# Optimization experiments

Measured on AMD Instinct MI355X. Metric: run time of the kernel, lower is better.

Reference implementation:

```python
import jax, jax.numpy as jnp
import numpy as np

D_MODEL = 1024
NUM_HEADS = 16
MAX_LEN = 500
D_K = D_MODEL // NUM_HEADS


def setup_inputs() -> dict:
    key = jax.random.key(0)
    ks = jax.random.split(key, 10)
    B, L = 8, 500
    s = 1.0 / np.sqrt(D_MODEL)
    return {
        "query": jax.random.normal(ks[0], (B, L, D_MODEL), dtype=jnp.float32),
        "key": jax.random.normal(ks[1], (B, L, D_MODEL), dtype=jnp.float32),
        "value": jax.random.normal(ks[2], (B, L, D_MODEL), dtype=jnp.float32),
        "Wq": jax.random.normal(ks[3], (D_MODEL, D_MODEL), dtype=jnp.float32) * s,
        "bq": jnp.zeros((D_MODEL,), dtype=jnp.float32),
        "Wk": jax.random.normal(ks[4], (D_MODEL, D_MODEL), dtype=jnp.float32) * s,
        "bk": jnp.zeros((D_MODEL,), dtype=jnp.float32),
        "Wv": jax.random.normal(ks[5], (D_MODEL, D_MODEL), dtype=jnp.float32) * s,
        "bv": jnp.zeros((D_MODEL,), dtype=jnp.float32),
        "rel_emb": jax.random.normal(ks[6], (NUM_HEADS, 2 * MAX_LEN - 1), dtype=jnp.float32),
    }


def reference(query, key, value, Wq, bq, Wk, bk, Wv, bv, rel_emb):
    B, Lq, _ = query.shape
    Lk = key.shape[1]
    H, dk = NUM_HEADS, D_K
    # QKV projections -> [B, H, L, d]
    q = (query @ Wq + bq).reshape(B, Lq, H, dk).transpose(0, 2, 1, 3)
    k = (key @ Wk + bk).reshape(B, Lk, H, dk).transpose(0, 2, 1, 3)
    v = (value @ Wv + bv).reshape(B, Lk, H, dk).transpose(0, 2, 1, 3)
    scores = jnp.einsum('bhqd,bhkd->bhqk', q, k) / jnp.sqrt(jnp.float32(dk))
    # gathered relative-position bias: [H, Lq, Lk]
    rel_idx = jnp.arange(Lq)[:, None] - jnp.arange(Lk)[None, :] + MAX_LEN - 1
    bias = rel_emb[:, rel_idx]  # [H, Lq, Lk]
    scores = scores + bias[None]
    attn = jax.nn.softmax(scores, axis=-1)
    out = jnp.einsum('bhqk,bhkd->bhqd', attn, v)
    return out.transpose(0, 2, 1, 3).reshape(B, Lq, H * dk)
```

## Files before the change

### kernel.cpp

```cpp
#include <hip/hip_runtime.h>

typedef short bf16x8 __attribute__((ext_vector_type(8)));
typedef float f32x4 __attribute__((ext_vector_type(4)));
typedef unsigned uint4v __attribute__((ext_vector_type(4)));

#define B_    8
#define L_    500
#define LP    512
#define H_    16
#define DK    64
#define DM    1024
#define MP    4096
#define NT    8

static __device__ __forceinline__ unsigned short f2bf(float x) {
  unsigned u = __float_as_uint(x);
  u += 0x7fffu + ((u >> 16) & 1u);
  return (unsigned short)(u >> 16);
}

static __device__ __forceinline__ unsigned cvtpk(float lo, float hi) {
  unsigned r;
  asm("v_cvt_pk_bf16_f32 %0, %1, %2" : "=v"(r) : "v"(lo), "v"(hi));
  return r;
}

static __device__ __forceinline__ void gload16(const void* g, void* l) {
  __builtin_amdgcn_global_load_lds(
      (const __attribute__((address_space(1))) void*)g,
      (__attribute__((address_space(3))) void*)l, 16, 0, 0);
}

static __device__ __forceinline__ f32x4 MF(bf16x8 a, bf16x8 b, f32x4 c) {
  return __builtin_amdgcn_mfma_f32_16x16x32_bf16(a, b, c, 0, 0, 0);
}

__global__ __launch_bounds__(256) void conv_kernel(
    const float* __restrict__ iq, const float* __restrict__ ik,
    const float* __restrict__ iv,
    const float* __restrict__ wq, const float* __restrict__ wk,
    const float* __restrict__ wv,
    unsigned short* __restrict__ X, unsigned short* __restrict__ Wt) {
  const int z = blockIdx.y;
  const int bx = blockIdx.x;
  const int tid = threadIdx.x;
  if (bx < 2048) {
    const float* src = (z == 0) ? iq : (z == 1) ? ik : iv;
    const size_t off = ((size_t)bx * 256 + tid) * 8;
    const int m = (int)(off >> 10);
    unsigned short o[8];
    if (m < 4000) {
      const float4 a = *(const float4*)(src + off);
      const float4 b = *(const float4*)(src + off + 4);
      o[0]=f2bf(a.x); o[1]=f2bf(a.y); o[2]=f2bf(a.z); o[3]=f2bf(a.w);
      o[4]=f2bf(b.x); o[5]=f2bf(b.y); o[6]=f2bf(b.z); o[7]=f2bf(b.w);
    } else {
#pragma unroll
      for (int i = 0; i < 8; ++i) o[i] = 0;
    }
    uint4 pk;
    pk.x = (unsigned)o[0] | ((unsigned)o[1] << 16);
    pk.y = (unsigned)o[2] | ((unsigned)o[3] << 16);
    pk.z = (unsigned)o[4] | ((unsigned)o[5] << 16);
    pk.w = (unsigned)o[6] | ((unsigned)o[7] << 16);
    *(uint4*)(X + (size_t)z * MP * DM + off) = pk;
    return;
  }
  const int bw = bx - 2048;
  const float* W = (z == 0) ? wq : (z == 1) ? wk : wv;
  const int k0 = (bw >> 4) * 64;
  const int n0 = (bw & 15) * 64;
  __shared__ float t[64][65];
  const int row = tid >> 2;
  const int cb  = (tid & 3) * 16;
#pragma unroll
  for (int s = 0; s < 4; ++s) {
    const float4 v = *(const float4*)(W + (size_t)(k0 + row) * DM + n0 + cb + s * 4);
    t[row][cb + s * 4 + 0] = v.x; t[row][cb + s * 4 + 1] = v.y;
    t[row][cb + s * 4 + 2] = v.z; t[row][cb + s * 4 + 3] = v.w;
  }
  __syncthreads();
  const int nr = tid >> 2;
  const int kb = (tid & 3) * 16;
#pragma unroll
  for (int s = 0; s < 2; ++s) {
    unsigned short o[8];
#pragma unroll
    for (int e = 0; e < 8; ++e) o[e] = f2bf(t[kb + s * 8 + e][nr]);
    uint4 pk;
    pk.x = (unsigned)o[0] | ((unsigned)o[1] << 16);
    pk.y = (unsigned)o[2] | ((unsigned)o[3] << 16);
    pk.z = (unsigned)o[4] | ((unsigned)o[5] << 16);
    pk.w = (unsigned)o[6] | ((unsigned)o[7] << 16);
    *(uint4*)(Wt + (size_t)z * DM * DM + (size_t)(n0 + nr) * DM + k0 + kb + s * 8) = pk;
  }
}

__global__ __launch_bounds__(256) void gemm_qkv_kernel(
    const unsigned short* __restrict__ X, const unsigned short* __restrict__ Wt,
    const float* __restrict__ bq, const float* __restrict__ bk,
    const float* __restrict__ bv,
    unsigned short* __restrict__ qo, unsigned short* __restrict__ ko,
    unsigned short* __restrict__ vo) {
  const int z = blockIdx.y;
  const unsigned short* A  = X  + (size_t)z * MP * DM;
  const unsigned short* Bw = Wt + (size_t)z * DM * DM;
  const float* bias = (z == 0) ? bq : (z == 1) ? bk : bv;
  unsigned short* out = (z == 0) ? qo : (z == 1) ? ko : vo;

  const int bid = blockIdx.x;
  const int xg = bid & 7, y = bid >> 3;
  const int tm = xg + 8 * (y >> 3);
  const int tn = y & 7;
  const int tid = threadIdx.x;
  const int lane = tid & 63, wid = tid >> 6;
  const int wr = wid >> 1, wc = wid & 1;
  const int lg = lane >> 4, lr = lane & 15;

  __shared__ __attribute__((aligned(16))) unsigned short sA[3][128 * 32];
  __shared__ __attribute__((aligned(16))) unsigned short sB[3][128 * 32];

  const int c0 = tid, c1 = tid + 256;
  const int ar0 = c0 >> 2, ak0 = (c0 & 3) * 8;
  const int ar1 = c1 >> 2, ak1 = (c1 & 3) * 8;
  const unsigned short* Ab = A  + (size_t)tm * 128 * DM;
  const unsigned short* Bb = Bw + (size_t)tn * 128 * DM;

  auto STAGE = [&](int t) {
    const int buf = t % 3;
    const int kn = t * 32;
    gload16(Ab + (size_t)ar0 * DM + kn + ak0, &sA[buf][c0 * 8]);
    gload16(Ab + (size_t)ar1 * DM + kn + ak1, &sA[buf][c1 * 8]);
    gload16(Bb + (size_t)ar0 * DM + kn + ak0, &sB[buf][c0 * 8]);
    gload16(Bb + (size_t)ar1 * DM + kn + ak1, &sB[buf][c1 * 8]);
  };

  f32x4 acc[4][4];
#pragma unroll
  for (int i = 0; i < 4; ++i)
#pragma unroll
    for (int j = 0; j < 4; ++j) acc[i][j] = (f32x4){0.f, 0.f, 0.f, 0.f};

  STAGE(0); STAGE(1);
  asm volatile("s_waitcnt vmcnt(4)" ::: "memory");
  __builtin_amdgcn_s_barrier();
  __builtin_amdgcn_sched_barrier(0);

  for (int t = 0; t < 32; ++t) {
    if (t < 30) STAGE(t + 2);
    const int cb = t % 3;
    bf16x8 af[4], bfr[4];
#pragma unroll
    for (int s = 0; s < 4; ++s) {
      af[s]  = *(const bf16x8*)&sA[cb][(wr * 64 + s * 16 + lr) * 32 + lg * 8];
      bfr[s] = *(const bf16x8*)&sB[cb][(wc * 64 + s * 16 + lr) * 32 + lg * 8];
    }
#pragma unroll
    for (int i = 0; i < 4; ++i)
#pragma unroll
      for (int j = 0; j < 4; ++j)
        acc[i][j] = MF(af[i], bfr[j], acc[i][j]);
    if (t < 31) {
      if (t < 30) asm volatile("s_waitcnt vmcnt(4)" ::: "memory");
      else        asm volatile("s_waitcnt vmcnt(0)" ::: "memory");
      __builtin_amdgcn_s_barrier();
      __builtin_amdgcn_sched_barrier(0);
    }
  }

  const int nbase = tn * 128 + wc * 64 + lr;
  float bias4[4];
#pragma unroll
  for (int ns = 0; ns < 4; ++ns) bias4[ns] = bias[nbase + ns * 16];

#pragma unroll
  for (int ms = 0; ms < 4; ++ms) {
#pragma unroll
    for (int r = 0; r < 4; ++r) {
      const int m = tm * 128 + wr * 64 + ms * 16 + lg * 4 + r;
      if (m < 4000) {
        const unsigned batch = (unsigned)m / 500u;
        const int lrow = m - (int)batch * 500;
#pragma unroll
        for (int ns = 0; ns < 4; ++ns) {
          const int n = nbase + ns * 16;
          const int hh = n >> 6, d = n & 63;
          out[(((size_t)batch * H_ + hh) * LP + lrow) * DK + d] =
              f2bf(acc[ms][ns][r] + bias4[ns]);
        }
      }
    }
  }
}

__global__ __launch_bounds__(256) void transpose_v_kernel(
    const unsigned short* __restrict__ v, unsigned short* __restrict__ vt) {
  const int bh = blockIdx.y;
  const int l0 = blockIdx.x * 64;
  __shared__ unsigned short t[64][72];
  const int tid = threadIdx.x;
  const int lrw = tid >> 2, dc = (tid & 3) * 16;
  const int gl = l0 + lrw;
  if (gl < L_) {
    *(uint4*)&t[lrw][dc]     = *(const uint4*)(v + ((size_t)bh * LP + gl) * DK + dc);
    *(uint4*)&t[lrw][dc + 8] = *(const uint4*)(v + ((size_t)bh * LP + gl) * DK + dc + 8);
  } else {
    const uint4 zz = {0u, 0u, 0u, 0u};
    *(uint4*)&t[lrw][dc]     = zz;
    *(uint4*)&t[lrw][dc + 8] = zz;
  }
  __syncthreads();
  const int dr = tid >> 2, lcb = (tid & 3) * 16;
#pragma unroll
  for (int s = 0; s < 2; ++s) {
    unsigned short e[8];
#pragma unroll
    for (int i = 0; i < 8; ++i) e[i] = t[lcb + s * 8 + i][dr];
    uint4 o;
    o.x = (unsigned)e[0] | ((unsigned)e[1] << 16);
    o.y = (unsigned)e[2] | ((unsigned)e[3] << 16);
    o.z = (unsigned)e[4] | ((unsigned)e[5] << 16);
    o.w = (unsigned)e[6] | ((unsigned)e[7] << 16);
    *(uint4*)(vt + ((size_t)bh * DK + dr) * LP + l0 + lcb + s * 8) = o;
  }
}

__global__ __launch_bounds__(256, 4) void attn_kernel(
    const unsigned short* __restrict__ q, const unsigned short* __restrict__ k,
    const unsigned short* __restrict__ vt, const float* __restrict__ rel,
    float* __restrict__ out) {
  const int id = blockIdx.x;
  const int bh = id & 127, qc = id >> 7;
  const int b = bh >> 4, h = bh & 15;
  const int tid = threadIdx.x;
  const int lane = tid & 63, wid = tid >> 6;
  const int lg = lane >> 4, lr = lane & 15;

  __shared__ unsigned short kt[2][2][64][32];
  __shared__ unsigned short vtt[2][2][64][32];
  __shared__ float relb[576];

  const float LOG2E = 1.44269504f;
  const float SC = 0.125f * LOG2E;
  const int rbase = qc * 64 - 12;
  for (int i = tid; i < 575; i += 256) {
    int idx = rbase + i;
    idx = idx < 0 ? 0 : (idx > 998 ? 998 : idx);
    relb[i] = rel[h * 999 + idx] * LOG2E;
  }

  const int qrow = qc * 64 + wid * 16 + lr;
  const unsigned short* qp = q + ((size_t)bh * LP + qrow) * DK + lg * 8;
  const bf16x8 qf0 = *(const bf16x8*)qp;
  const bf16x8 qf1 = *(const bf16x8*)(qp + 32);

  const int kj = tid >> 2, dc = (tid & 3) * 16;
  const unsigned short* kgp = k + ((size_t)bh * LP + kj) * DK + dc;
  unsigned short* kls = &kt[0][dc >> 5][kj][dc & 31];
  const int vd = tid >> 2, vkg = (tid & 3) * 16;
  const unsigned short* vgp = vt + ((size_t)bh * DK + vd) * LP + vkg;
  unsigned short* vls = &vtt[0][vkg >> 5][vd][vkg & 31];

  const int sig0 = 8 * (lr >> 2) + (lr & 3);
  const int qin = wid * 16 + lr;

  f32x4 o[4];
#pragma unroll
  for (int d = 0; d < 4; ++d) o[d] = (f32x4){0.f, 0.f, 0.f, 0.f};
  float mrun = -1e30f, lrun = 0.f;

  uint4 ka0 = *(const uint4*)(kgp);
  uint4 ka1 = *(const uint4*)(kgp + 8);
  uint4 va0 = *(const uint4*)(vgp);
  uint4 va1 = *(const uint4*)(vgp + 8);

  for (int t = 0; t < NT; ++t) {
    const int buf = t & 1;
    *(uint4*)(kls + buf * 4096)     = ka0;
    *(uint4*)(kls + buf * 4096 + 8) = ka1;
    *(uint4*)(vls + buf * 4096)     = va0;
    *(uint4*)(vls + buf * 4096 + 8) = va1;
    __syncthreads();

    if (t < NT - 1) {
      const size_t ko_ = (size_t)(t + 1) * 64 * DK;
      ka0 = *(const uint4*)(kgp + ko_);
      ka1 = *(const uint4*)(kgp + ko_ + 8);
      va0 = *(const uint4*)(vgp + (t + 1) * 64);
      va1 = *(const uint4*)(vgp + (t + 1) * 64 + 8);
    }

    f32x4 s[2][2];
#pragma unroll
    for (int kc = 0; kc < 2; ++kc)
#pragma unroll
      for (int hf = 0; hf < 2; ++hf) {
        const int sg = kc * 32 + hf * 4 + sig0;
        const bf16x8 a0 = *(const bf16x8*)&kt[buf][0][sg][lg * 8];
        const bf16x8 a1 = *(const bf16x8*)&kt[buf][1][sg][lg * 8];
        f32x4 ss = (f32x4){0.f, 0.f, 0.f, 0.f};
        ss = __builtin_amdgcn_mfma_f32_16x16x32_bf16(a0, qf0, ss, 0, 0, 0);
        ss = __builtin_amdgcn_mfma_f32_16x16x32_bf16(a1, qf1, ss, 0, 0, 0);
        s[kc][hf] = ss;
      }

    float sc[2][2][4];
#pragma unroll
    for (int kc = 0; kc < 2; ++kc)
#pragma unroll
      for (int hf = 0; hf < 2; ++hf) {
        const int bidx = qin - (t * 64 + kc * 32 + 8 * lg + 4 * hf) + 511;
#pragma unroll
        for (int r = 0; r < 4; ++r)
          sc[kc][hf][r] = s[kc][hf][r] * SC + relb[bidx - r];
      }
    if (t == NT - 1) {
#pragma unroll
      for (int hf = 0; hf < 2; ++hf)
#pragma unroll
        for (int r = 0; r < 4; ++r)
          if (8 * lg + 4 * hf + r >= 20) sc[1][hf][r] = -1e30f;
    }

    float m0 = fmaxf(fmaxf(sc[0][0][0], sc[0][0][1]), fmaxf(sc[0][0][2], sc[0][0][3]));
    float m1 = fmaxf(fmaxf(sc[0][1][0], sc[0][1][1]), fmaxf(sc[0][1][2], sc[0][1][3]));
    float m2 = fmaxf(fmaxf(sc[1][0][0], sc[1][0][1]), fmaxf(sc[1][0][2], sc[1][0][3]));
    float m3 = fmaxf(fmaxf(sc[1][1][0], sc[1][1][1]), fmaxf(sc[1][1][2], sc[1][1][3]));
    const float mloc = fmaxf(fmaxf(m0, m1), fmaxf(m2, m3));
    if (!__all(mloc - mrun <= 11.5f)) {
      float mx = fmaxf(mloc, mrun);
      mx = fmaxf(mx, __shfl_xor(mx, 16));
      mx = fmaxf(mx, __shfl_xor(mx, 32));
      const float alpha = exp2f(mrun - mx);
      mrun = mx;
      lrun *= alpha;
#pragma unroll
      for (int d = 0; d < 4; ++d) {
        o[d][0] *= alpha; o[d][1] *= alpha; o[d][2] *= alpha; o[d][3] *= alpha;
      }
    }

    float rs = 0.f;
    unsigned pw[2][4];
#pragma unroll
    for (int kc = 0; kc < 2; ++kc)
#pragma unroll
      for (int hf = 0; hf < 2; ++hf) {
        float p0 = exp2f(sc[kc][hf][0] - mrun);
        float p1 = exp2f(sc[kc][hf][1] - mrun);
        float p2 = exp2f(sc[kc][hf][2] - mrun);
        float p3 = exp2f(sc[kc][hf][3] - mrun);
        rs += (p0 + p1) + (p2 + p3);
        pw[kc][hf * 2 + 0] = cvtpk(p0, p1);
        pw[kc][hf * 2 + 1] = cvtpk(p2, p3);
      }
    rs += __shfl_xor(rs, 16);
    rs += __shfl_xor(rs, 32);
    lrun += rs;

#pragma unroll
    for (int kc = 0; kc < 2; ++kc) {
      union { uint4v u; bf16x8 v; } cv;
      cv.u = (uint4v){pw[kc][0], pw[kc][1], pw[kc][2], pw[kc][3]};
      const bf16x8 pf = cv.v;
#pragma unroll
      for (int db = 0; db < 4; ++db) {
        const bf16x8 vf = *(const bf16x8*)&vtt[buf][kc][db * 16 + lr][lg * 8];
        o[db] = __builtin_amdgcn_mfma_f32_16x16x32_bf16(vf, pf, o[db], 0, 0, 0);
      }
    }
  }

  if (qrow < L_) {
    const float inv = 1.0f / lrun;
    float* op = out + ((size_t)b * L_ + qrow) * DM + h * DK + lg * 4;
#pragma unroll
    for (int db = 0; db < 4; ++db) {
      float4 v;
      v.x = o[db][0] * inv; v.y = o[db][1] * inv;
      v.z = o[db][2] * inv; v.w = o[db][3] * inv;
      *(float4*)(op + db * 16) = v;
    }
  }
}

extern "C" void kernel_launch(void* const* d_in, const int* in_sizes, int n_in,
                              void* d_out, int out_size, void* d_ws, size_t ws_size,
                              hipStream_t stream) {
  const float* iq  = (const float*)d_in[0];
  const float* ik  = (const float*)d_in[1];
  const float* iv  = (const float*)d_in[2];
  const float* wq  = (const float*)d_in[3];
  const float* bq  = (const float*)d_in[4];
  const float* wk  = (const float*)d_in[5];
  const float* bk  = (const float*)d_in[6];
  const float* wv  = (const float*)d_in[7];
  const float* bv  = (const float*)d_in[8];
  const float* rel = (const float*)d_in[9];
  float* out = (float*)d_out;

  char* w = (char*)d_ws;
  unsigned short* X   = (unsigned short*)(w);
  unsigned short* Wt  = (unsigned short*)(w + 25165824);
  unsigned short* qb  = (unsigned short*)(w + 31457280);
  unsigned short* kb  = (unsigned short*)(w + 39845888);
  unsigned short* vb  = (unsigned short*)(w + 48234496);
  unsigned short* vtb = (unsigned short*)(w + 56623104);

  conv_kernel<<<dim3(2304, 3), 256, 0, stream>>>(iq, ik, iv, wq, wk, wv, X, Wt);
  gemm_qkv_kernel<<<dim3(256, 3), 256, 0, stream>>>(X, Wt, bq, bk, bv, qb, kb, vb);
  transpose_v_kernel<<<dim3(8, 128), 256, 0, stream>>>(vb, vtb);
  attn_kernel<<<1024, 256, 0, stream>>>(qb, kb, vtb, rel, out);
}
```

Measured before the change: 88.99 us.

## Unroll GEMM ring buffer by three and double attention query tile per block

```diff
diff --git a/kernel.cpp b/kernel.cpp
--- a/kernel.cpp
+++ b/kernel.cpp
@@ -96,6 +96,31 @@
   }
 }
 
+#define GSTEP(T_, BUF_, NBUF_)                                                    \
+  {                                                                               \
+    if ((T_) < 30) {                                                              \
+      const int kn_ = ((T_) + 2) * 32;                                            \
+      gload16(gA0 + kn_, &sA[NBUF_][c0 * 8]);                                     \
+      gload16(gA1 + kn_, &sA[NBUF_][c1 * 8]);                                     \
+      gload16(gB0 + kn_, &sB[NBUF_][c0 * 8]);                                     \
+      gload16(gB1 + kn_, &sB[NBUF_][c1 * 8]);                                     \
+    }                                                                             \
+    bf16x8 af[4], bfr[4];                                                         \
+    _Pragma("unroll") for (int s = 0; s < 4; ++s) {                               \
+      af[s]  = *(const bf16x8*)&sA[BUF_][(wr * 64 + s * 16 + lr) * 32 + lg * 8];  \
+      bfr[s] = *(const bf16x8*)&sB[BUF_][(wc * 64 + s * 16 + lr) * 32 + lg * 8];  \
+    }                                                                             \
+    _Pragma("unroll") for (int i = 0; i < 4; ++i)                                 \
+      _Pragma("unroll") for (int j = 0; j < 4; ++j)                               \
+        acc[i][j] = MF(af[i], bfr[j], acc[i][j]);                                 \
+    if ((T_) < 31) {                                                              \
+      if ((T_) < 30) asm volatile("s_waitcnt vmcnt(4)" ::: "memory");             \
+      else           asm volatile("s_waitcnt vmcnt(0)" ::: "memory");             \
+      __builtin_amdgcn_s_barrier();                                               \
+      __builtin_amdgcn_sched_barrier(0);                                          \
+    }                                                                             \
+  }
+
 __global__ __launch_bounds__(256) void gemm_qkv_kernel(
     const unsigned short* __restrict__ X, const unsigned short* __restrict__ Wt,
     const float* __restrict__ bq, const float* __restrict__ bk,
@@ -125,15 +150,10 @@
   const int ar1 = c1 >> 2, ak1 = (c1 & 3) * 8;
   const unsigned short* Ab = A  + (size_t)tm * 128 * DM;
   const unsigned short* Bb = Bw + (size_t)tn * 128 * DM;
-
-  auto STAGE = [&](int t) {
-    const int buf = t % 3;
-    const int kn = t * 32;
-    gload16(Ab + (size_t)ar0 * DM + kn + ak0, &sA[buf][c0 * 8]);
-    gload16(Ab + (size_t)ar1 * DM + kn + ak1, &sA[buf][c1 * 8]);
-    gload16(Bb + (size_t)ar0 * DM + kn + ak0, &sB[buf][c0 * 8]);
-    gload16(Bb + (size_t)ar1 * DM + kn + ak1, &sB[buf][c1 * 8]);
-  };
+  const unsigned short* gA0 = Ab + (size_t)ar0 * DM + ak0;
+  const unsigned short* gA1 = Ab + (size_t)ar1 * DM + ak1;
+  const unsigned short* gB0 = Bb + (size_t)ar0 * DM + ak0;
+  const unsigned short* gB1 = Bb + (size_t)ar1 * DM + ak1;
 
   f32x4 acc[4][4];
 #pragma unroll
@@ -141,32 +161,25 @@
 #pragma unroll
     for (int j = 0; j < 4; ++j) acc[i][j] = (f32x4){0.f, 0.f, 0.f, 0.f};
 
-  STAGE(0); STAGE(1);
+  gload16(gA0, &sA[0][c0 * 8]);
+  gload16(gA1, &sA[0][c1 * 8]);
+  gload16(gB0, &sB[0][c0 * 8]);
+  gload16(gB1, &sB[0][c1 * 8]);
+  gload16(gA0 + 32, &sA[1][c0 * 8]);
+  gload16(gA1 + 32, &sA[1][c1 * 8]);
+  gload16(gB0 + 32, &sB[1][c0 * 8]);
+  gload16(gB1 + 32, &sB[1][c1 * 8]);
   asm volatile("s_waitcnt vmcnt(4)" ::: "memory");
   __builtin_amdgcn_s_barrier();
   __builtin_amdgcn_sched_barrier(0);
 
-  for (int t = 0; t < 32; ++t) {
-    if (t < 30) STAGE(t + 2);
-    const int cb = t % 3;
-    bf16x8 af[4], bfr[4];
-#pragma unroll
-    for (int s = 0; s < 4; ++s) {
-      af[s]  = *(const bf16x8*)&sA[cb][(wr * 64 + s * 16 + lr) * 32 + lg * 8];
-      bfr[s] = *(const bf16x8*)&sB[cb][(wc * 64 + s * 16 + lr) * 32 + lg * 8];
-    }
-#pragma unroll
-    for (int i = 0; i < 4; ++i)
-#pragma unroll
-      for (int j = 0; j < 4; ++j)
-        acc[i][j] = MF(af[i], bfr[j], acc[i][j]);
-    if (t < 31) {
-      if (t < 30) asm volatile("s_waitcnt vmcnt(4)" ::: "memory");
-      else        asm volatile("s_waitcnt vmcnt(0)" ::: "memory");
-      __builtin_amdgcn_s_barrier();
-      __builtin_amdgcn_sched_barrier(0);
-    }
-  }
+  for (int t = 0; t < 30; t += 3) {
+    GSTEP(t,     0, 2);
+    GSTEP(t + 1, 1, 0);
+    GSTEP(t + 2, 2, 1);
+  }
+  GSTEP(30, 0, 2);
+  GSTEP(31, 1, 0);
 
   const int nbase = tn * 128 + wc * 64 + lr;
   float bias4[4];
@@ -225,7 +238,7 @@
   }
 }
 
-__global__ __launch_bounds__(256, 4) void attn_kernel(
+__global__ __launch_bounds__(512, 2) void attn_kernel(
     const unsigned short* __restrict__ q, const unsigned short* __restrict__ k,
     const unsigned short* __restrict__ vt, const float* __restrict__ rel,
     float* __restrict__ out) {
@@ -238,26 +251,26 @@
 
   __shared__ unsigned short kt[2][2][64][32];
   __shared__ unsigned short vtt[2][2][64][32];
-  __shared__ float relb[576];
+  __shared__ float relb[640];
 
   const float LOG2E = 1.44269504f;
   const float SC = 0.125f * LOG2E;
-  const int rbase = qc * 64 - 12;
-  for (int i = tid; i < 575; i += 256) {
+  const int rbase = qc * 128 - 12;
+  for (int i = tid; i < 639; i += 512) {
     int idx = rbase + i;
     idx = idx < 0 ? 0 : (idx > 998 ? 998 : idx);
     relb[i] = rel[h * 999 + idx] * LOG2E;
   }
 
-  const int qrow = qc * 64 + wid * 16 + lr;
+  const int qrow = qc * 128 + wid * 16 + lr;
   const unsigned short* qp = q + ((size_t)bh * LP + qrow) * DK + lg * 8;
   const bf16x8 qf0 = *(const bf16x8*)qp;
   const bf16x8 qf1 = *(const bf16x8*)(qp + 32);
 
-  const int kj = tid >> 2, dc = (tid & 3) * 16;
-  const unsigned short* kgp = k + ((size_t)bh * LP + kj) * DK + dc;
-  unsigned short* kls = &kt[0][dc >> 5][kj][dc & 31];
-  const int vd = tid >> 2, vkg = (tid & 3) * 16;
+  const int kj = tid >> 3, dcs = (tid & 7) * 8;
+  const unsigned short* kgp = k + ((size_t)bh * LP + kj) * DK + dcs;
+  unsigned short* kls = &kt[0][dcs >> 5][kj][dcs & 31];
+  const int vd = tid >> 3, vkg = (tid & 7) * 8;
   const unsigned short* vgp = vt + ((size_t)bh * DK + vd) * LP + vkg;
   unsigned short* vls = &vtt[0][vkg >> 5][vd][vkg & 31];
 
@@ -270,24 +283,17 @@
   float mrun = -1e30f, lrun = 0.f;
 
   uint4 ka0 = *(const uint4*)(kgp);
-  uint4 ka1 = *(const uint4*)(kgp + 8);
   uint4 va0 = *(const uint4*)(vgp);
-  uint4 va1 = *(const uint4*)(vgp + 8);
 
   for (int t = 0; t < NT; ++t) {
     const int buf = t & 1;
-    *(uint4*)(kls + buf * 4096)     = ka0;
-    *(uint4*)(kls + buf * 4096 + 8) = ka1;
-    *(uint4*)(vls + buf * 4096)     = va0;
-    *(uint4*)(vls + buf * 4096 + 8) = va1;
+    *(uint4*)(kls + buf * 4096) = ka0;
+    *(uint4*)(vls + buf * 4096) = va0;
     __syncthreads();
 
     if (t < NT - 1) {
-      const size_t ko_ = (size_t)(t + 1) * 64 * DK;
-      ka0 = *(const uint4*)(kgp + ko_);
-      ka1 = *(const uint4*)(kgp + ko_ + 8);
+      ka0 = *(const uint4*)(kgp + (size_t)(t + 1) * 64 * DK);
       va0 = *(const uint4*)(vgp + (t + 1) * 64);
-      va1 = *(const uint4*)(vgp + (t + 1) * 64 + 8);
     }
 
     f32x4 s[2][2];
@@ -410,5 +416,5 @@
   conv_kernel<<<dim3(2304, 3), 256, 0, stream>>>(iq, ik, iv, wq, wk, wv, X, Wt);
   gemm_qkv_kernel<<<dim3(256, 3), 256, 0, stream>>>(X, Wt, bq, bk, bv, qb, kb, vb);
   transpose_v_kernel<<<dim3(8, 128), 256, 0, stream>>>(vb, vtb);
-  attn_kernel<<<1024, 256, 0, stream>>>(qb, kb, vtb, rel, out);
-}
+  attn_kernel<<<512, 512, 0, stream>>>(qb, kb, vtb, rel, out);
+}
```

Result: slower. 95.23 us (+7.0%).

## Fuse V transpose into QKV GEMM epilogue and enlarge attention blocks

Applied to the files above, without the earlier changes.

```diff
diff --git a/kernel.cpp b/kernel.cpp
--- a/kernel.cpp
+++ b/kernel.cpp
@@ -40,7 +40,8 @@
     const float* __restrict__ iv,
     const float* __restrict__ wq, const float* __restrict__ wk,
     const float* __restrict__ wv,
-    unsigned short* __restrict__ X, unsigned short* __restrict__ Wt) {
+    unsigned short* __restrict__ X, unsigned short* __restrict__ Wt,
+    unsigned short* __restrict__ vt) {
   const int z = blockIdx.y;
   const int bx = blockIdx.x;
   const int tid = threadIdx.x;
@@ -66,6 +67,16 @@
     *(uint4*)(X + (size_t)z * MP * DM + off) = pk;
     return;
   }
+  if (bx >= 2304) {
+    if (z == 0) {
+      const int idx = (bx - 2304) * 256 + tid;
+      unsigned short* p = vt + (size_t)idx * LP + 496;
+      const uint4 zz = {0u, 0u, 0u, 0u};
+      *(uint4*)(p)     = zz;
+      *(uint4*)(p + 8) = zz;
+    }
+    return;
+  }
   const int bw = bx - 2048;
   const float* W = (z == 0) ? wq : (z == 1) ? wk : wv;
   const int k0 = (bw >> 4) * 64;
@@ -173,59 +184,49 @@
 #pragma unroll
   for (int ns = 0; ns < 4; ++ns) bias4[ns] = bias[nbase + ns * 16];
 
-#pragma unroll
-  for (int ms = 0; ms < 4; ++ms) {
-#pragma unroll
-    for (int r = 0; r < 4; ++r) {
-      const int m = tm * 128 + wr * 64 + ms * 16 + lg * 4 + r;
-      if (m < 4000) {
-        const unsigned batch = (unsigned)m / 500u;
-        const int lrow = m - (int)batch * 500;
+  if (z == 2) {
+#pragma unroll
+    for (int ms = 0; ms < 4; ++ms) {
+      const int m0 = tm * 128 + wr * 64 + ms * 16 + lg * 4;
+      if (m0 < 4000) {
+        const unsigned batch = (unsigned)m0 / 500u;
+        const int lrow0 = m0 - (int)batch * 500;
 #pragma unroll
         for (int ns = 0; ns < 4; ++ns) {
           const int n = nbase + ns * 16;
           const int hh = n >> 6, d = n & 63;
-          out[(((size_t)batch * H_ + hh) * LP + lrow) * DK + d] =
-              f2bf(acc[ms][ns][r] + bias4[ns]);
+          uint2 pk;
+          pk.x = (unsigned)f2bf(acc[ms][ns][0] + bias4[ns]) |
+                 ((unsigned)f2bf(acc[ms][ns][1] + bias4[ns]) << 16);
+          pk.y = (unsigned)f2bf(acc[ms][ns][2] + bias4[ns]) |
+                 ((unsigned)f2bf(acc[ms][ns][3] + bias4[ns]) << 16);
+          *(uint2*)(out + (((size_t)batch * H_ + hh) * DK + d) * LP + lrow0) = pk;
         }
       }
     }
-  }
-}
-
-__global__ __launch_bounds__(256) void transpose_v_kernel(
-    const unsigned short* __restrict__ v, unsigned short* __restrict__ vt) {
-  const int bh = blockIdx.y;
-  const int l0 = blockIdx.x * 64;
-  __shared__ unsigned short t[64][72];
-  const int tid = threadIdx.x;
-  const int lrw = tid >> 2, dc = (tid & 3) * 16;
-  const int gl = l0 + lrw;
-  if (gl < L_) {
-    *(uint4*)&t[lrw][dc]     = *(const uint4*)(v + ((size_t)bh * LP + gl) * DK + dc);
-    *(uint4*)&t[lrw][dc + 8] = *(const uint4*)(v + ((size_t)bh * LP + gl) * DK + dc + 8);
   } else {
-    const uint4 zz = {0u, 0u, 0u, 0u};
-    *(uint4*)&t[lrw][dc]     = zz;
-    *(uint4*)&t[lrw][dc + 8] = zz;
-  }
-  __syncthreads();
-  const int dr = tid >> 2, lcb = (tid & 3) * 16;
-#pragma unroll
-  for (int s = 0; s < 2; ++s) {
-    unsigned short e[8];
-#pragma unroll
-    for (int i = 0; i < 8; ++i) e[i] = t[lcb + s * 8 + i][dr];
-    uint4 o;
-    o.x = (unsigned)e[0] | ((unsigned)e[1] << 16);
-    o.y = (unsigned)e[2] | ((unsigned)e[3] << 16);
-    o.z = (unsigned)e[4] | ((unsigned)e[5] << 16);
-    o.w = (unsigned)e[6] | ((unsigned)e[7] << 16);
-    *(uint4*)(vt + ((size_t)bh * DK + dr) * LP + l0 + lcb + s * 8) = o;
-  }
-}
-
-__global__ __launch_bounds__(256, 4) void attn_kernel(
+#pragma unroll
+    for (int ms = 0; ms < 4; ++ms) {
+#pragma unroll
+      for (int r = 0; r < 4; ++r) {
+        const int m = tm * 128 + wr * 64 + ms * 16 + lg * 4 + r;
+        if (m < 4000) {
+          const unsigned batch = (unsigned)m / 500u;
+          const int lrow = m - (int)batch * 500;
+#pragma unroll
+          for (int ns = 0; ns < 4; ++ns) {
+            const int n = nbase + ns * 16;
+            const int hh = n >> 6, d = n & 63;
+            out[(((size_t)batch * H_ + hh) * LP + lrow) * DK + d] =
+                f2bf(acc[ms][ns][r] + bias4[ns]);
+          }
+        }
+      }
+    }
+  }
+}
+
+__global__ __launch_bounds__(512, 2) void attn_kernel(
     const unsigned short* __restrict__ q, const unsigned short* __restrict__ k,
     const unsigned short* __restrict__ vt, const float* __restrict__ rel,
     float* __restrict__ out) {
@@ -238,26 +239,26 @@
 
   __shared__ unsigned short kt[2][2][64][32];
   __shared__ unsigned short vtt[2][2][64][32];
-  __shared__ float relb[576];
+  __shared__ float relb[640];
 
   const float LOG2E = 1.44269504f;
   const float SC = 0.125f * LOG2E;
-  const int rbase = qc * 64 - 12;
-  for (int i = tid; i < 575; i += 256) {
+  const int rbase = qc * 128 - 12;
+  for (int i = tid; i < 639; i += 512) {
     int idx = rbase + i;
     idx = idx < 0 ? 0 : (idx > 998 ? 998 : idx);
     relb[i] = rel[h * 999 + idx] * LOG2E;
   }
 
-  const int qrow = qc * 64 + wid * 16 + lr;
+  const int qrow = qc * 128 + wid * 16 + lr;
   const unsigned short* qp = q + ((size_t)bh * LP + qrow) * DK + lg * 8;
   const bf16x8 qf0 = *(const bf16x8*)qp;
   const bf16x8 qf1 = *(const bf16x8*)(qp + 32);
 
-  const int kj = tid >> 2, dc = (tid & 3) * 16;
-  const unsigned short* kgp = k + ((size_t)bh * LP + kj) * DK + dc;
-  unsigned short* kls = &kt[0][dc >> 5][kj][dc & 31];
-  const int vd = tid >> 2, vkg = (tid & 3) * 16;
+  const int kj = tid >> 3, dcs = (tid & 7) * 8;
+  const unsigned short* kgp = k + ((size_t)bh * LP + kj) * DK + dcs;
+  unsigned short* kls = &kt[0][dcs >> 5][kj][dcs & 31];
+  const int vd = tid >> 3, vkg = (tid & 7) * 8;
   const unsigned short* vgp = vt + ((size_t)bh * DK + vd) * LP + vkg;
   unsigned short* vls = &vtt[0][vkg >> 5][vd][vkg & 31];
 
@@ -270,24 +271,17 @@
   float mrun = -1e30f, lrun = 0.f;
 
   uint4 ka0 = *(const uint4*)(kgp);
-  uint4 ka1 = *(const uint4*)(kgp + 8);
   uint4 va0 = *(const uint4*)(vgp);
-  uint4 va1 = *(const uint4*)(vgp + 8);
 
   for (int t = 0; t < NT; ++t) {
     const int buf = t & 1;
-    *(uint4*)(kls + buf * 4096)     = ka0;
-    *(uint4*)(kls + buf * 4096 + 8) = ka1;
-    *(uint4*)(vls + buf * 4096)     = va0;
-    *(uint4*)(vls + buf * 4096 + 8) = va1;
+    *(uint4*)(kls + buf * 4096) = ka0;
+    *(uint4*)(vls + buf * 4096) = va0;
     __syncthreads();
 
     if (t < NT - 1) {
-      const size_t ko_ = (size_t)(t + 1) * 64 * DK;
-      ka0 = *(const uint4*)(kgp + ko_);
-      ka1 = *(const uint4*)(kgp + ko_ + 8);
+      ka0 = *(const uint4*)(kgp + (size_t)(t + 1) * 64 * DK);
       va0 = *(const uint4*)(vgp + (t + 1) * 64);
-      va1 = *(const uint4*)(vgp + (t + 1) * 64 + 8);
     }
 
     f32x4 s[2][2];
@@ -404,11 +398,9 @@
   unsigned short* Wt  = (unsigned short*)(w + 25165824);
   unsigned short* qb  = (unsigned short*)(w + 31457280);
   unsigned short* kb  = (unsigned short*)(w + 39845888);
-  unsigned short* vb  = (unsigned short*)(w + 48234496);
-  unsigned short* vtb = (unsigned short*)(w + 56623104);
-
-  conv_kernel<<<dim3(2304, 3), 256, 0, stream>>>(iq, ik, iv, wq, wk, wv, X, Wt);
-  gemm_qkv_kernel<<<dim3(256, 3), 256, 0, stream>>>(X, Wt, bq, bk, bv, qb, kb, vb);
-  transpose_v_kernel<<<dim3(8, 128), 256, 0, stream>>>(vb, vtb);
-  attn_kernel<<<1024, 256, 0, stream>>>(qb, kb, vtb, rel, out);
-}
+  unsigned short* vtb = (unsigned short*)(w + 48234496);
+
+  conv_kernel<<<dim3(2336, 3), 256, 0, stream>>>(iq, ik, iv, wq, wk, wv, X, Wt, vtb);
+  gemm_qkv_kernel<<<dim3(256, 3), 256, 0, stream>>>(X, Wt, bq, bk, bv, qb, kb, vtb);
+  attn_kernel<<<512, 512, 0, stream>>>(qb, kb, vtb, rel, out);
+}
```

Result: faster. 84.30 us (-5.3%).
